# Kernel optimization log

Measured on AMD Instinct MI355X. Metric: run time of the kernel, lower is better.

## Reference

```python
import jax, jax.numpy as jnp
import numpy as np

N_NODES = 100000
N_EDGES = 1600000
D_IN = 256
H = 4       # n_heads
F = 64      # out_feats per head
NEG_SLOPE = 0.2


def setup_inputs() -> dict:
    key = jax.random.key(0)
    ks = jax.random.split(key, 8)
    feat = jax.random.normal(ks[0], (N_NODES, D_IN), dtype=jnp.float32)
    src = jax.random.randint(ks[1], (N_EDGES,), 0, N_NODES, dtype=jnp.int32)
    dst = jnp.sort(jax.random.randint(ks[2], (N_EDGES,), 0, N_NODES, dtype=jnp.int32))
    s = 1.0 / np.sqrt(D_IN)
    W_src = jax.random.normal(ks[3], (D_IN, H * F), dtype=jnp.float32) * s
    W_dst = jax.random.normal(ks[4], (D_IN, H * F), dtype=jnp.float32) * s
    b_dst = jnp.zeros((H * F,), dtype=jnp.float32)
    Wa_src = jax.random.normal(ks[5], (D_IN, H), dtype=jnp.float32) * s
    Wa_dst = jax.random.normal(ks[6], (D_IN, H), dtype=jnp.float32) * s
    return {"feat": feat, "W_src": W_src, "W_dst": W_dst, "b_dst": b_dst,
            "Wa_src": Wa_src, "Wa_dst": Wa_dst, "src": src, "dst": dst}


def reference(feat, W_src, W_dst, b_dst, Wa_src, Wa_dst, src, dst):
    N = feat.shape[0]
    # node projections
    h_src = (feat @ W_src).reshape(N, H, F)                  # [N,H,F]
    h_dst = (feat @ W_dst + b_dst).reshape(N, H, F)          # residual term
    a_src = feat @ Wa_src                                    # [N,H]
    a_dst = feat @ Wa_dst                                    # [N,H]
    # per-edge attention logits: u_add_v then leaky_relu
    e = a_src[src] + a_dst[dst]                              # [E,H]
    e = jnp.where(e > 0, e, NEG_SLOPE * e)
    # edge softmax grouped by destination node
    emax = jax.ops.segment_max(e, dst, num_segments=N)       # [N,H]
    emax = jnp.where(jnp.isfinite(emax), emax, 0.0)          # empty segments -> 0
    ex = jnp.exp(e - emax[dst])                              # [E,H]
    denom = jax.ops.segment_sum(ex, dst, num_segments=N)     # [N,H]
    a = ex / denom[dst]                                      # [E,H]
    # u_mul_e + sum aggregation
    msg = h_src[src] * a[:, :, None]                         # [E,H,F]
    out = jax.ops.segment_sum(msg, dst, num_segments=N)      # [N,H,F]
    return out + h_dst
```

## Files before the change

kernel.cpp:

```cpp
#include <hip/hip_runtime.h>

#define N_NODES 100000
#define N_EDGES 1600000
#define NEG_SLOPE 0.2f

typedef __bf16 bf16x8 __attribute__((ext_vector_type(8)));
typedef float f32x4 __attribute__((ext_vector_type(4)));
typedef _Float16 f16x4 __attribute__((ext_vector_type(4)));

__device__ inline unsigned short f2bf(float f) {
    union { float f; unsigned u; } x; x.f = f;
    unsigned r = x.u + 0x7fffu + ((x.u >> 16) & 1u);
    return (unsigned short)(r >> 16);
}

__global__ __launch_bounds__(256) void cvt_w_k(const float* __restrict__ Ws,
                                               const float* __restrict__ Wd,
                                               unsigned short* __restrict__ Wsw_src,
                                               unsigned short* __restrict__ Wsw_dst) {
    int idx = blockIdx.x * 256 + threadIdx.x;
    int sel = idx >> 16;
    int r = idx & 65535;
    int k = r >> 8, n = r & 255;
    int ct = n >> 4, nl = n & 15;
    int lane = ((k & 31) >> 3) * 16 + nl, j = k & 7;
    int ks = k >> 5;
    unsigned short v = f2bf((sel == 0 ? Ws : Wd)[k * 256 + n]);
    (sel == 0 ? Wsw_src : Wsw_dst)[(ct * 8 + ks) * 512 + lane * 8 + j] = v;
}

__global__ void cvt_wa_k(const float* __restrict__ Was,
                         const float* __restrict__ Wad,
                         unsigned short* __restrict__ Wa_sw) {
    int idx = blockIdx.x * 256 + threadIdx.x;
    int j = idx & 7, lane = (idx >> 3) & 63, ks = idx >> 9;
    int n = lane & 15, k = ks * 32 + (lane >> 4) * 8 + j;
    float v = n < 4 ? Was[k * 4 + n] : (n < 8 ? Wad[k * 4 + (n - 4)] : 0.f);
    Wa_sw[idx] = f2bf(v);
}

__global__ void rowptr_k(const int* __restrict__ dst, int* __restrict__ rp) {
    int n = blockIdx.x * 256 + threadIdx.x;
    if (n > N_NODES) return;
    int lo = 0, hi = N_EDGES;
    while (lo < hi) { int mid = (lo + hi) >> 1; if (dst[mid] < n) lo = mid + 1; else hi = mid; }
    rp[n] = lo;
}

__global__ __launch_bounds__(256) void aproj_k(const float* __restrict__ feat,
                                               const unsigned short* __restrict__ Wa_sw,
                                               _Float16* __restrict__ a_srcH,
                                               _Float16* __restrict__ a_dstH) {
    int wave = threadIdx.x >> 6, lane = threadIdx.x & 63;
    int quad = lane >> 4, l16 = lane & 15;
    int row_strip = (blockIdx.x * 4 + wave) * 16;
    int arow = row_strip + l16;
    if (arow >= N_NODES) arow = N_NODES - 1;
    const float* arow_p = feat + (size_t)arow * 256;
    const bf16x8* Wa8 = (const bf16x8*)Wa_sw;
    f32x4 acc = {0.f, 0.f, 0.f, 0.f};
    #pragma unroll
    for (int ks = 0; ks < 8; ++ks) {
        int k0 = ks * 32 + quad * 8;
        float4 f0 = *(const float4*)(arow_p + k0);
        float4 f1 = *(const float4*)(arow_p + k0 + 4);
        union { unsigned short u[8]; bf16x8 v; } cv;
        cv.u[0] = f2bf(f0.x); cv.u[1] = f2bf(f0.y);
        cv.u[2] = f2bf(f0.z); cv.u[3] = f2bf(f0.w);
        cv.u[4] = f2bf(f1.x); cv.u[5] = f2bf(f1.y);
        cv.u[6] = f2bf(f1.z); cv.u[7] = f2bf(f1.w);
        acc = __builtin_amdgcn_mfma_f32_16x16x32_bf16(cv.v, Wa8[ks * 64 + lane], acc, 0, 0, 0);
    }
    #pragma unroll
    for (int r = 0; r < 4; ++r) {
        int n = row_strip + quad * 4 + r;
        if (n < N_NODES) {
            if (l16 < 4)      a_srcH[(size_t)n * 4 + l16] = (_Float16)acc[r];
            else if (l16 < 8) a_dstH[(size_t)n * 4 + (l16 - 4)] = (_Float16)acc[r];
        }
    }
}

__global__ __launch_bounds__(512) void proj_k(const float* __restrict__ feat,
                                              const unsigned short* __restrict__ Wsw_src,
                                              const unsigned short* __restrict__ Wsw_dst,
                                              const float* __restrict__ b_dst,
                                              _Float16* __restrict__ h_src,
                                              float* __restrict__ out) {
    __shared__ unsigned short F[4 * 32 * 17 * 8];
    int tid = threadIdx.x, wave = tid >> 6, lane = tid & 63;
    int quad = lane >> 4, l16 = lane & 15;
    int base = blockIdx.x * 64;

    #pragma unroll
    for (int it = 0; it < 8; ++it) {
        int c = tid + it * 512;
        int m = c >> 6, k0 = (c & 63) * 4;
        int row = base + m; if (row > N_NODES - 1) row = N_NODES - 1;
        float4 f = *(const float4*)(feat + (size_t)row * 256 + k0);
        ushort4 u;
        u.x = f2bf(f.x); u.y = f2bf(f.y); u.z = f2bf(f.z); u.w = f2bf(f.w);
        int strip = m >> 4, ms = m & 15, kq = k0 >> 3, jb = k0 & 7;
        *(ushort4*)&F[((strip * 32 + kq) * 17 + ms) * 8 + jb] = u;
    }
    __syncthreads();

    bool isSrc = wave < 4;
    int cg = (wave & 3) * 4;
    const bf16x8* W8 = (const bf16x8*)(isSrc ? Wsw_src : Wsw_dst);

    f32x4 acc[4][4];
    #pragma unroll
    for (int s = 0; s < 4; ++s)
        #pragma unroll
        for (int c = 0; c < 4; ++c) acc[s][c] = (f32x4){0.f, 0.f, 0.f, 0.f};

    #pragma unroll
    for (int ks = 0; ks < 8; ++ks) {
        bf16x8 B0 = W8[((cg + 0) * 8 + ks) * 64 + lane];
        bf16x8 B1 = W8[((cg + 1) * 8 + ks) * 64 + lane];
        bf16x8 B2 = W8[((cg + 2) * 8 + ks) * 64 + lane];
        bf16x8 B3 = W8[((cg + 3) * 8 + ks) * 64 + lane];
        #pragma unroll
        for (int s = 0; s < 4; ++s) {
            bf16x8 A = *(const bf16x8*)&F[((s * 32 + ks * 4 + quad) * 17 + l16) * 8];
            acc[s][0] = __builtin_amdgcn_mfma_f32_16x16x32_bf16(A, B0, acc[s][0], 0, 0, 0);
            acc[s][1] = __builtin_amdgcn_mfma_f32_16x16x32_bf16(A, B1, acc[s][1], 0, 0, 0);
            acc[s][2] = __builtin_amdgcn_mfma_f32_16x16x32_bf16(A, B2, acc[s][2], 0, 0, 0);
            acc[s][3] = __builtin_amdgcn_mfma_f32_16x16x32_bf16(A, B3, acc[s][3], 0, 0, 0);
        }
    }

    if (isSrc) {
        #pragma unroll
        for (int s = 0; s < 4; ++s)
            #pragma unroll
            for (int c = 0; c < 4; ++c) {
                int col = (cg + c) * 16 + l16;
                #pragma unroll
                for (int r = 0; r < 4; ++r) {
                    int row = base + s * 16 + quad * 4 + r;
                    if (row < N_NODES)
                        h_src[(size_t)row * 256 + col] = (_Float16)acc[s][c][r];
                }
            }
    } else {
        #pragma unroll
        for (int c = 0; c < 4; ++c) {
            int col = (cg + c) * 16 + l16;
            float b = b_dst[col];
            #pragma unroll
            for (int s = 0; s < 4; ++s)
                #pragma unroll
                for (int r = 0; r < 4; ++r) {
                    int row = base + s * 16 + quad * 4 + r;
                    if (row < N_NODES)
                        out[(size_t)row * 256 + col] = acc[s][c][r] + b;
                }
        }
    }
}

__global__ __launch_bounds__(256, 6) void agg2_k(const int* __restrict__ src,
                                                 const int* __restrict__ rp,
                                                 const _Float16* __restrict__ a_srcH,
                                                 const _Float16* __restrict__ a_dstH,
                                                 const _Float16* __restrict__ h_src,
                                                 float* __restrict__ out) {
    __shared__ float WT[4][64][4];
    int tid = threadIdx.x, wave = tid >> 6, lane = tid & 63;
    int node = blockIdx.x * 4 + wave;
    int head = lane >> 4;
    int r0 = rp[node], r1 = rp[node + 1], deg = r1 - r0;

    size_t o = (size_t)node * 256 + lane * 4;
    float4 pv = *(const float4*)(out + o);

    f32x4 g = (f32x4){0.f, 0.f, 0.f, 0.f};
    const _Float16* hl = h_src + lane * 4;

    if (deg > 0 && deg <= 64) {
        f16x4 adv4 = *(const f16x4*)(a_dstH + (size_t)node * 4);
        float ad0 = (float)adv4[0], ad1 = (float)adv4[1];
        float ad2 = (float)adv4[2], ad3 = (float)adv4[3];
        bool act = lane < deg;
        int s = 0;
        f16x4 av4 = (f16x4){0, 0, 0, 0};
        if (act) {
            s = src[r0 + lane];
            av4 = *(const f16x4*)(a_srcH + (size_t)s * 4);
        }
        float e0 = (float)av4[0] + ad0; e0 = e0 > 0.f ? e0 : NEG_SLOPE * e0;
        float e1 = (float)av4[1] + ad1; e1 = e1 > 0.f ? e1 : NEG_SLOPE * e1;
        float e2 = (float)av4[2] + ad2; e2 = e2 > 0.f ? e2 : NEG_SLOPE * e2;
        float e3 = (float)av4[3] + ad3; e3 = e3 > 0.f ? e3 : NEG_SLOPE * e3;
        if (!act) { e0 = e1 = e2 = e3 = -1e30f; }
        float m0 = e0, m1 = e1, m2 = e2, m3 = e3;
        for (int off = 1; off < deg; off <<= 1) {
            m0 = fmaxf(m0, __shfl_xor(m0, off));
            m1 = fmaxf(m1, __shfl_xor(m1, off));
            m2 = fmaxf(m2, __shfl_xor(m2, off));
            m3 = fmaxf(m3, __shfl_xor(m3, off));
        }
        float w0 = act ? __expf(e0 - m0) : 0.f;
        float w1 = act ? __expf(e1 - m1) : 0.f;
        float w2 = act ? __expf(e2 - m2) : 0.f;
        float w3 = act ? __expf(e3 - m3) : 0.f;
        float d0 = w0, d1 = w1, d2 = w2, d3 = w3;
        for (int off = 1; off < deg; off <<= 1) {
            d0 += __shfl_xor(d0, off); d1 += __shfl_xor(d1, off);
            d2 += __shfl_xor(d2, off); d3 += __shfl_xor(d3, off);
        }
        w0 *= 1.f / d0; w1 *= 1.f / d1; w2 *= 1.f / d2; w3 *= 1.f / d3;
        float4 wv; wv.x = w0; wv.y = w1; wv.z = w2; wv.w = w3;
        *(float4*)&WT[wave][lane][0] = wv;
        asm volatile("s_waitcnt lgkmcnt(0)" ::: "memory");

        int j = 0;
        for (; j + 4 <= deg; j += 4) {
            int s0 = __builtin_amdgcn_readlane(s, j);
            int s1 = __builtin_amdgcn_readlane(s, j + 1);
            int s2 = __builtin_amdgcn_readlane(s, j + 2);
            int s3 = __builtin_amdgcn_readlane(s, j + 3);
            f16x4 h0 = *(const f16x4*)(hl + (size_t)s0 * 256);
            f16x4 h1 = *(const f16x4*)(hl + (size_t)s1 * 256);
            f16x4 h2 = *(const f16x4*)(hl + (size_t)s2 * 256);
            f16x4 h3 = *(const f16x4*)(hl + (size_t)s3 * 256);
            float x0 = WT[wave][j][head],     x1 = WT[wave][j + 1][head];
            float x2 = WT[wave][j + 2][head], x3 = WT[wave][j + 3][head];
            g[0] += x0 * (float)h0[0]; g[1] += x0 * (float)h0[1];
            g[2] += x0 * (float)h0[2]; g[3] += x0 * (float)h0[3];
            g[0] += x1 * (float)h1[0]; g[1] += x1 * (float)h1[1];
            g[2] += x1 * (float)h1[2]; g[3] += x1 * (float)h1[3];
            g[0] += x2 * (float)h2[0]; g[1] += x2 * (float)h2[1];
            g[2] += x2 * (float)h2[2]; g[3] += x2 * (float)h2[3];
            g[0] += x3 * (float)h3[0]; g[1] += x3 * (float)h3[1];
            g[2] += x3 * (float)h3[2]; g[3] += x3 * (float)h3[3];
        }
        for (; j < deg; ++j) {
            int sj = __builtin_amdgcn_readlane(s, j);
            float xj = WT[wave][j][head];
            f16x4 h = *(const f16x4*)(hl + (size_t)sj * 256);
            g[0] += xj * (float)h[0]; g[1] += xj * (float)h[1];
            g[2] += xj * (float)h[2]; g[3] += xj * (float)h[3];
        }
    } else if (deg > 64) {
        f16x4 adv4 = *(const f16x4*)(a_dstH + (size_t)node * 4);
        float ad0 = (float)adv4[0], ad1 = (float)adv4[1];
        float ad2 = (float)adv4[2], ad3 = (float)adv4[3];
        float m0 = -1e30f, m1 = -1e30f, m2 = -1e30f, m3 = -1e30f;
        for (int e = r0 + lane; e < r1; e += 64) {
            int se = src[e];
            f16x4 av4 = *(const f16x4*)(a_srcH + (size_t)se * 4);
            float e0 = (float)av4[0] + ad0; e0 = e0 > 0.f ? e0 : NEG_SLOPE * e0;
            float e1 = (float)av4[1] + ad1; e1 = e1 > 0.f ? e1 : NEG_SLOPE * e1;
            float e2 = (float)av4[2] + ad2; e2 = e2 > 0.f ? e2 : NEG_SLOPE * e2;
            float e3 = (float)av4[3] + ad3; e3 = e3 > 0.f ? e3 : NEG_SLOPE * e3;
            m0 = fmaxf(m0, e0); m1 = fmaxf(m1, e1);
            m2 = fmaxf(m2, e2); m3 = fmaxf(m3, e3);
        }
        #pragma unroll
        for (int off = 32; off > 0; off >>= 1) {
            m0 = fmaxf(m0, __shfl_xor(m0, off)); m1 = fmaxf(m1, __shfl_xor(m1, off));
            m2 = fmaxf(m2, __shfl_xor(m2, off)); m3 = fmaxf(m3, __shfl_xor(m3, off));
        }
        float d0 = 0.f, d1 = 0.f, d2 = 0.f, d3 = 0.f;
        for (int e = r0 + lane; e < r1; e += 64) {
            int se = src[e];
            f16x4 av4 = *(const f16x4*)(a_srcH + (size_t)se * 4);
            float e0 = (float)av4[0] + ad0; e0 = e0 > 0.f ? e0 : NEG_SLOPE * e0;
            float e1 = (float)av4[1] + ad1; e1 = e1 > 0.f ? e1 : NEG_SLOPE * e1;
            float e2 = (float)av4[2] + ad2; e2 = e2 > 0.f ? e2 : NEG_SLOPE * e2;
            float e3 = (float)av4[3] + ad3; e3 = e3 > 0.f ? e3 : NEG_SLOPE * e3;
            d0 += __expf(e0 - m0); d1 += __expf(e1 - m1);
            d2 += __expf(e2 - m2); d3 += __expf(e3 - m3);
        }
        #pragma unroll
        for (int off = 32; off > 0; off >>= 1) {
            d0 += __shfl_xor(d0, off); d1 += __shfl_xor(d1, off);
            d2 += __shfl_xor(d2, off); d3 += __shfl_xor(d3, off);
        }
        float i0 = 1.f / d0, i1 = 1.f / d1, i2 = 1.f / d2, i3 = 1.f / d3;
        for (int c0 = r0; c0 < r1; c0 += 64) {
            int cnt = min(64, r1 - c0);
            int s = 0; float w0 = 0.f, w1 = 0.f, w2 = 0.f, w3 = 0.f;
            if (lane < cnt) {
                s = src[c0 + lane];
                f16x4 av4 = *(const f16x4*)(a_srcH + (size_t)s * 4);
                float e0 = (float)av4[0] + ad0; e0 = e0 > 0.f ? e0 : NEG_SLOPE * e0;
                float e1 = (float)av4[1] + ad1; e1 = e1 > 0.f ? e1 : NEG_SLOPE * e1;
                float e2 = (float)av4[2] + ad2; e2 = e2 > 0.f ? e2 : NEG_SLOPE * e2;
                float e3 = (float)av4[3] + ad3; e3 = e3 > 0.f ? e3 : NEG_SLOPE * e3;
                w0 = __expf(e0 - m0) * i0; w1 = __expf(e1 - m1) * i1;
                w2 = __expf(e2 - m2) * i2; w3 = __expf(e3 - m3) * i3;
            }
            float4 wv; wv.x = w0; wv.y = w1; wv.z = w2; wv.w = w3;
            *(float4*)&WT[wave][lane][0] = wv;
            asm volatile("s_waitcnt lgkmcnt(0)" ::: "memory");
            for (int j = 0; j < cnt; ++j) {
                int sj = __builtin_amdgcn_readlane(s, j);
                float xj = WT[wave][j][head];
                f16x4 h = *(const f16x4*)(hl + (size_t)sj * 256);
                g[0] += xj * (float)h[0]; g[1] += xj * (float)h[1];
                g[2] += xj * (float)h[2]; g[3] += xj * (float)h[3];
            }
        }
    }
    float4 res;
    res.x = pv.x + g[0]; res.y = pv.y + g[1];
    res.z = pv.z + g[2]; res.w = pv.w + g[3];
    *(float4*)(out + o) = res;
}

extern "C" void kernel_launch(void* const* d_in, const int* in_sizes, int n_in,
                              void* d_out, int out_size, void* d_ws, size_t ws_size,
                              hipStream_t stream) {
    const float* feat   = (const float*)d_in[0];
    const float* W_src  = (const float*)d_in[1];
    const float* W_dst  = (const float*)d_in[2];
    const float* b_dst  = (const float*)d_in[3];
    const float* Wa_src = (const float*)d_in[4];
    const float* Wa_dst = (const float*)d_in[5];
    const int*   src    = (const int*)d_in[6];
    const int*   dst    = (const int*)d_in[7];
    float* out = (float*)d_out;
    char* ws = (char*)d_ws;

    _Float16* h_srcH        = (_Float16*)(ws);
    unsigned short* Wsw_src = (unsigned short*)(ws + 51200000);
    unsigned short* Wsw_dst = (unsigned short*)(ws + 51331072);
    unsigned short* Wa_sw   = (unsigned short*)(ws + 51462144);
    _Float16* a_srcH        = (_Float16*)(ws + 51470336);
    _Float16* a_dstH        = (_Float16*)(ws + 52270336);
    int*      rp            = (int*)(ws + 53070336);

    hipLaunchKernelGGL(cvt_w_k,  dim3(512),   dim3(256), 0, stream, W_src, W_dst, Wsw_src, Wsw_dst);
    hipLaunchKernelGGL(cvt_wa_k, dim3(16),    dim3(256), 0, stream, Wa_src, Wa_dst, Wa_sw);
    hipLaunchKernelGGL(rowptr_k, dim3(391),   dim3(256), 0, stream, dst, rp);
    hipLaunchKernelGGL(aproj_k,  dim3(1563),  dim3(256), 0, stream, feat, Wa_sw, a_srcH, a_dstH);
    hipLaunchKernelGGL(proj_k,   dim3(1563),  dim3(512), 0, stream, feat, Wsw_src, Wsw_dst,
                       b_dst, h_srcH, out);
    hipLaunchKernelGGL(agg2_k,   dim3(25000), dim3(256), 0, stream, src, rp, a_srcH, a_dstH,
                       h_srcH, out);
}
```

Measured before the change: 419.3 us.

## Merge prep kernels, unroll gather loop by eight, raise agg occupancy bound

Three small setup kernels (weight swizzle, attention-weight swizzle, row pointer binary search) are fused into one launch with block-range dispatch, removing two kernel launches. The aggregation kernel gains an 8-way unrolled gather loop so more independent h_src loads are in flight per wave. Its launch bound also moves from 6 to 8 waves per SIMD, which may constrain registers and cause spills.

```diff
diff --git a/kernel.cpp b/kernel.cpp
--- a/kernel.cpp
+++ b/kernel.cpp
@@ -14,37 +14,39 @@
     return (unsigned short)(r >> 16);
 }
 
-__global__ __launch_bounds__(256) void cvt_w_k(const float* __restrict__ Ws,
-                                               const float* __restrict__ Wd,
-                                               unsigned short* __restrict__ Wsw_src,
-                                               unsigned short* __restrict__ Wsw_dst) {
-    int idx = blockIdx.x * 256 + threadIdx.x;
-    int sel = idx >> 16;
-    int r = idx & 65535;
-    int k = r >> 8, n = r & 255;
-    int ct = n >> 4, nl = n & 15;
-    int lane = ((k & 31) >> 3) * 16 + nl, j = k & 7;
-    int ks = k >> 5;
-    unsigned short v = f2bf((sel == 0 ? Ws : Wd)[k * 256 + n]);
-    (sel == 0 ? Wsw_src : Wsw_dst)[(ct * 8 + ks) * 512 + lane * 8 + j] = v;
-}
-
-__global__ void cvt_wa_k(const float* __restrict__ Was,
-                         const float* __restrict__ Wad,
-                         unsigned short* __restrict__ Wa_sw) {
-    int idx = blockIdx.x * 256 + threadIdx.x;
-    int j = idx & 7, lane = (idx >> 3) & 63, ks = idx >> 9;
-    int n = lane & 15, k = ks * 32 + (lane >> 4) * 8 + j;
-    float v = n < 4 ? Was[k * 4 + n] : (n < 8 ? Wad[k * 4 + (n - 4)] : 0.f);
-    Wa_sw[idx] = f2bf(v);
-}
-
-__global__ void rowptr_k(const int* __restrict__ dst, int* __restrict__ rp) {
-    int n = blockIdx.x * 256 + threadIdx.x;
-    if (n > N_NODES) return;
-    int lo = 0, hi = N_EDGES;
-    while (lo < hi) { int mid = (lo + hi) >> 1; if (dst[mid] < n) lo = mid + 1; else hi = mid; }
-    rp[n] = lo;
+__global__ __launch_bounds__(256) void prep_k(const float* __restrict__ Ws,
+                                              const float* __restrict__ Wd,
+                                              const float* __restrict__ Was,
+                                              const float* __restrict__ Wad,
+                                              const int* __restrict__ dst,
+                                              unsigned short* __restrict__ Wsw_src,
+                                              unsigned short* __restrict__ Wsw_dst,
+                                              unsigned short* __restrict__ Wa_sw,
+                                              int* __restrict__ rp) {
+    int b = blockIdx.x;
+    if (b < 512) {
+        int idx = b * 256 + threadIdx.x;
+        int sel = idx >> 16;
+        int r = idx & 65535;
+        int k = r >> 8, n = r & 255;
+        int ct = n >> 4, nl = n & 15;
+        int lane = ((k & 31) >> 3) * 16 + nl, j = k & 7;
+        int ks = k >> 5;
+        unsigned short v = f2bf((sel == 0 ? Ws : Wd)[k * 256 + n]);
+        (sel == 0 ? Wsw_src : Wsw_dst)[(ct * 8 + ks) * 512 + lane * 8 + j] = v;
+    } else if (b < 528) {
+        int idx = (b - 512) * 256 + threadIdx.x;
+        int j = idx & 7, lane = (idx >> 3) & 63, ks = idx >> 9;
+        int n = lane & 15, k = ks * 32 + (lane >> 4) * 8 + j;
+        float v = n < 4 ? Was[k * 4 + n] : (n < 8 ? Wad[k * 4 + (n - 4)] : 0.f);
+        Wa_sw[idx] = f2bf(v);
+    } else {
+        int n = (b - 528) * 256 + threadIdx.x;
+        if (n > N_NODES) return;
+        int lo = 0, hi = N_EDGES;
+        while (lo < hi) { int mid = (lo + hi) >> 1; if (dst[mid] < n) lo = mid + 1; else hi = mid; }
+        rp[n] = lo;
+    }
 }
 
 __global__ __launch_bounds__(256) void aproj_k(const float* __restrict__ feat,
@@ -161,7 +163,7 @@
     }
 }
 
-__global__ __launch_bounds__(256, 6) void agg2_k(const int* __restrict__ src,
+__global__ __launch_bounds__(256, 8) void agg2_k(const int* __restrict__ src,
                                                  const int* __restrict__ rp,
                                                  const _Float16* __restrict__ a_srcH,
                                                  const _Float16* __restrict__ a_dstH,
@@ -217,6 +219,44 @@
         asm volatile("s_waitcnt lgkmcnt(0)" ::: "memory");
 
         int j = 0;
+        for (; j + 8 <= deg; j += 8) {
+            int s0 = __builtin_amdgcn_readlane(s, j);
+            int s1 = __builtin_amdgcn_readlane(s, j + 1);
+            int s2 = __builtin_amdgcn_readlane(s, j + 2);
+            int s3 = __builtin_amdgcn_readlane(s, j + 3);
+            int s4 = __builtin_amdgcn_readlane(s, j + 4);
+            int s5 = __builtin_amdgcn_readlane(s, j + 5);
+            int s6 = __builtin_amdgcn_readlane(s, j + 6);
+            int s7 = __builtin_amdgcn_readlane(s, j + 7);
+            f16x4 h0 = *(const f16x4*)(hl + (size_t)s0 * 256);
+            f16x4 h1 = *(const f16x4*)(hl + (size_t)s1 * 256);
+            f16x4 h2 = *(const f16x4*)(hl + (size_t)s2 * 256);
+            f16x4 h3 = *(const f16x4*)(hl + (size_t)s3 * 256);
+            f16x4 h4 = *(const f16x4*)(hl + (size_t)s4 * 256);
+            f16x4 h5 = *(const f16x4*)(hl + (size_t)s5 * 256);
+            f16x4 h6 = *(const f16x4*)(hl + (size_t)s6 * 256);
+            f16x4 h7 = *(const f16x4*)(hl + (size_t)s7 * 256);
+            float x0 = WT[wave][j][head],     x1 = WT[wave][j + 1][head];
+            float x2 = WT[wave][j + 2][head], x3 = WT[wave][j + 3][head];
+            float x4 = WT[wave][j + 4][head], x5 = WT[wave][j + 5][head];
+            float x6 = WT[wave][j + 6][head], x7 = WT[wave][j + 7][head];
+            g[0] += x0 * (float)h0[0]; g[1] += x0 * (float)h0[1];
+            g[2] += x0 * (float)h0[2]; g[3] += x0 * (float)h0[3];
+            g[0] += x1 * (float)h1[0]; g[1] += x1 * (float)h1[1];
+            g[2] += x1 * (float)h1[2]; g[3] += x1 * (float)h1[3];
+            g[0] += x2 * (float)h2[0]; g[1] += x2 * (float)h2[1];
+            g[2] += x2 * (float)h2[2]; g[3] += x2 * (float)h2[3];
+            g[0] += x3 * (float)h3[0]; g[1] += x3 * (float)h3[1];
+            g[2] += x3 * (float)h3[2]; g[3] += x3 * (float)h3[3];
+            g[0] += x4 * (float)h4[0]; g[1] += x4 * (float)h4[1];
+            g[2] += x4 * (float)h4[2]; g[3] += x4 * (float)h4[3];
+            g[0] += x5 * (float)h5[0]; g[1] += x5 * (float)h5[1];
+            g[2] += x5 * (float)h5[2]; g[3] += x5 * (float)h5[3];
+            g[0] += x6 * (float)h6[0]; g[1] += x6 * (float)h6[1];
+            g[2] += x6 * (float)h6[2]; g[3] += x6 * (float)h6[3];
+            g[0] += x7 * (float)h7[0]; g[1] += x7 * (float)h7[1];
+            g[2] += x7 * (float)h7[2]; g[3] += x7 * (float)h7[3];
+        }
         for (; j + 4 <= deg; j += 4) {
             int s0 = __builtin_amdgcn_readlane(s, j);
             int s1 = __builtin_amdgcn_readlane(s, j + 1);
@@ -334,12 +374,11 @@
     _Float16* a_dstH        = (_Float16*)(ws + 52270336);
     int*      rp            = (int*)(ws + 53070336);
 
-    hipLaunchKernelGGL(cvt_w_k,  dim3(512),   dim3(256), 0, stream, W_src, W_dst, Wsw_src, Wsw_dst);
-    hipLaunchKernelGGL(cvt_wa_k, dim3(16),    dim3(256), 0, stream, Wa_src, Wa_dst, Wa_sw);
-    hipLaunchKernelGGL(rowptr_k, dim3(391),   dim3(256), 0, stream, dst, rp);
-    hipLaunchKernelGGL(aproj_k,  dim3(1563),  dim3(256), 0, stream, feat, Wa_sw, a_srcH, a_dstH);
-    hipLaunchKernelGGL(proj_k,   dim3(1563),  dim3(512), 0, stream, feat, Wsw_src, Wsw_dst,
+    hipLaunchKernelGGL(prep_k,  dim3(919),   dim3(256), 0, stream, W_src, W_dst, Wa_src, Wa_dst,
+                       dst, Wsw_src, Wsw_dst, Wa_sw, rp);
+    hipLaunchKernelGGL(aproj_k, dim3(1563),  dim3(256), 0, stream, feat, Wa_sw, a_srcH, a_dstH);
+    hipLaunchKernelGGL(proj_k,  dim3(1563),  dim3(512), 0, stream, feat, Wsw_src, Wsw_dst,
                        b_dst, h_srcH, out);
-    hipLaunchKernelGGL(agg2_k,   dim3(25000), dim3(256), 0, stream, src, rp, a_srcH, a_dstH,
+    hipLaunchKernelGGL(agg2_k,  dim3(25000), dim3(256), 0, stream, src, rp, a_srcH, a_dstH,
                        h_srcH, out);
 }
```

Measured after the change: 430.3 us. 1.03x slower.
